# Kernel tuning notes

Hardware: AMD Instinct MI355X
Metric: run time of the kernel (lower is better)

## Reference

```python
import jax, jax.numpy as jnp
import numpy as np

NUM_HEADS = 6
HEAD_SIZE = 64
N_EMBD = 384


def setup_inputs() -> dict:
    key = jax.random.key(0)
    k1, k2, k3 = jax.random.split(key, 3)
    B, T, C = 256, 256, N_EMBD
    x = jax.random.normal(k1, (B, T, C), dtype=jnp.float32)
    # torch Linear(n_embd, 3*n_embd, bias=False): y = x @ W.T; store transposed for x @ W
    W_qkv = jax.random.normal(k2, (C, 3 * C), dtype=jnp.float32) * (1.0 / np.sqrt(C))
    W_proj = jax.random.normal(k3, (C, C), dtype=jnp.float32) * (1.0 / np.sqrt(C))
    b_proj = jnp.zeros((C,), dtype=jnp.float32)
    return {"x": x, "W_qkv": W_qkv, "W_proj": W_proj, "b_proj": b_proj}


def reference(x, W_qkv, W_proj, b_proj):
    B, T, C = x.shape
    H, D = NUM_HEADS, HEAD_SIZE
    qkv = x @ W_qkv                                  # [B, T, 3C]
    q, k, v = jnp.split(qkv, 3, axis=-1)
    # [B, T, C] -> [B, H, T, D]
    q = q.reshape(B, T, H, D).transpose(0, 2, 1, 3)
    k = k.reshape(B, T, H, D).transpose(0, 2, 1, 3)
    v = v.reshape(B, T, H, D).transpose(0, 2, 1, 3)
    att = jnp.einsum("bhtd,bhsd->bhts", q, k) / np.sqrt(D).astype(jnp.float32)
    causal = jnp.tril(jnp.ones((T, T), dtype=bool))  # tril buffer
    att = jnp.where(causal[None, None], att, -jnp.inf)
    att = jax.nn.softmax(att, axis=-1)
    # dropout layers are identity in eval mode
    out = jnp.einsum("bhts,bhsd->bhtd", att, v)      # [B, H, T, D]
    out = out.transpose(0, 2, 1, 3).reshape(B, T, C)
    return out @ W_proj.T @ jnp.eye(C, dtype=out.dtype) if False else out @ W_proj + b_proj
```

## Files before the change

### kernel.cpp

```cpp
#include <hip/hip_runtime.h>
#include <hip/hip_bf16.h>
#include <stdint.h>

typedef __hip_bfloat16 bf16;
using f32x4 = __attribute__((ext_vector_type(4))) float;
using s16x8 = __attribute__((ext_vector_type(8))) short;

#define MFMA16(A_, B_, C_) __builtin_amdgcn_mfma_f32_16x16x32_bf16((A_), (B_), (C_), 0, 0, 0)

__device__ __forceinline__ void gload16(const void* g, void* l) {
  __builtin_amdgcn_global_load_lds((const __attribute__((address_space(1))) void*)g,
                                   (__attribute__((address_space(3))) void*)l, 16, 0, 0);
}

__global__ __launch_bounds__(256) void detect_kernel(const void* __restrict__ x,
                                                     int* __restrict__ flag) {
  __shared__ int cnt;
  if (threadIdx.x == 0) cnt = 0;
  __syncthreads();
  const uint32_t* w = (const uint32_t*)x;
  int local = 0;
#pragma unroll
  for (int i = 0; i < 8; ++i) {
    uint32_t v = w[threadIdx.x * 8 + i];
    uint32_t e = (v >> 7) & 0xFF;
    if (e >= 110 && e <= 135) local++;
  }
  atomicAdd(&cnt, local);
  __syncthreads();
  if (threadIdx.x == 0) *flag = (cnt < 1024) ? 1 : 0;
}

__global__ __launch_bounds__(256) void convert_kernel(const void* __restrict__ x,
                                                      bf16* __restrict__ xb,
                                                      size_t elem_off,
                                                      const int* __restrict__ flag) {
  size_t i = ((size_t)blockIdx.x * 256 + threadIdx.x) * 8;
  if (*flag) {
    const float* xf = (const float*)x + elem_off + i;
    float4 a = ((const float4*)xf)[0];
    float4 b = ((const float4*)xf)[1];
    union { bf16 h[8]; uint4 u; } o;
    o.h[0] = __float2bfloat16(a.x); o.h[1] = __float2bfloat16(a.y);
    o.h[2] = __float2bfloat16(a.z); o.h[3] = __float2bfloat16(a.w);
    o.h[4] = __float2bfloat16(b.x); o.h[5] = __float2bfloat16(b.y);
    o.h[6] = __float2bfloat16(b.z); o.h[7] = __float2bfloat16(b.w);
    *(uint4*)(&xb[i]) = o.u;
  } else {
    *(uint4*)(&xb[i]) = *(const uint4*)((const bf16*)x + elem_off + i);
  }
}

__global__ __launch_bounds__(256) void transpose_kernel(const void* __restrict__ W,
                                                        bf16* __restrict__ Wt,
                                                        int K, int N,
                                                        const int* __restrict__ flag) {
  int idx = blockIdx.x * 256 + threadIdx.x;
  if (idx >= K * N) return;
  int n = idx / K;
  int k = idx - n * K;
  if (*flag)
    Wt[idx] = __float2bfloat16(((const float*)W)[k * N + n]);
  else
    Wt[idx] = ((const bf16*)W)[k * N + n];
}

template <int MODE>
__global__ __launch_bounds__(256) void gemm_kernel(
    const bf16* __restrict__ A, const bf16* __restrict__ Bt,
    bf16* __restrict__ qb, bf16* __restrict__ kb, bf16* __restrict__ vb,
    void* __restrict__ outp, const void* __restrict__ bias,
    int r_off, const int* __restrict__ flag) {
  constexpr int K = 384;
  __shared__ bf16 Ash[128 * 32];
  __shared__ bf16 Bsh[128 * 32];
  const int tid = threadIdx.x;
  const int lane = tid & 63;
  const int wave = tid >> 6;
  const int wm = wave & 1, wn = wave >> 1;
  const int l15 = lane & 15, quad = lane >> 4;
  const int n0 = blockIdx.x * 128, m0 = blockIdx.y * 128;

  const int rl = lane >> 2;
  const int slot = lane & 3;
  const int sc = (slot - (lane >> 3)) & 3;
  const size_t lane_goff = (size_t)rl * K + sc * 8;

  const int arow0 = wave * 32;
  const bf16* Ag0 = A + (size_t)(m0 + arow0) * K + lane_goff;
  const bf16* Ag1 = Ag0 + (size_t)16 * K;
  const bf16* Bg0 = Bt + (size_t)(n0 + arow0) * K + lane_goff;
  const bf16* Bg1 = Bg0 + (size_t)16 * K;
  bf16* Al0 = &Ash[arow0 * 32];
  bf16* Al1 = &Ash[(arow0 + 16) * 32];
  bf16* Bl0 = &Bsh[arow0 * 32];
  bf16* Bl1 = &Bsh[(arow0 + 16) * 32];

  const int fc = ((quad + (l15 >> 1)) & 3) * 8;

  const f32x4 z4 = {0.f, 0.f, 0.f, 0.f};
  f32x4 acc[4][4];
#pragma unroll
  for (int i = 0; i < 4; ++i)
#pragma unroll
    for (int j = 0; j < 4; ++j) acc[i][j] = z4;

  for (int kt = 0; kt < 12; ++kt) {
    const int k0 = kt * 32;
    gload16(Ag0 + k0, Al0);
    gload16(Ag1 + k0, Al1);
    gload16(Bg0 + k0, Bl0);
    gload16(Bg1 + k0, Bl1);
    __syncthreads();
    s16x8 af[4], bfr[4];
#pragma unroll
    for (int i = 0; i < 4; ++i) {
      af[i] = *(const s16x8*)(&Ash[(wm * 64 + i * 16 + l15) * 32 + fc]);
      bfr[i] = *(const s16x8*)(&Bsh[(wn * 64 + i * 16 + l15) * 32 + fc]);
    }
#pragma unroll
    for (int i = 0; i < 4; ++i)
#pragma unroll
      for (int j = 0; j < 4; ++j) acc[i][j] = MFMA16(af[i], bfr[j], acc[i][j]);
    __syncthreads();
  }

  const int mbase = m0 + wm * 64;
  const int nbase = n0 + wn * 64;
  if (MODE == 0) {
    const int sel = blockIdx.x / 3;
    bf16* dst = (sel == 0) ? qb : ((sel == 1) ? kb : vb);
#pragma unroll
    for (int i = 0; i < 4; ++i) {
#pragma unroll
      for (int j = 0; j < 4; ++j) {
        int n_g = nbase + j * 16 + l15;
        int c = n_g - sel * 384;
        int h = c >> 6, d = c & 63;
#pragma unroll
        for (int r = 0; r < 4; ++r) {
          int m_loc = mbase + i * 16 + quad * 4 + r;
          int b = m_loc >> 8, t = m_loc & 255;
          bf16 bv = __float2bfloat16(acc[i][j][r]);
          int bh = b * 6 + h;
          if (sel < 2)
            dst[(size_t)bh * 16384 + t * 64 + d] = bv;
          else
            dst[(size_t)bh * 16384 + d * 256 + t] = bv;
        }
      }
    }
  } else {
    const int f32io = *flag;
#pragma unroll
    for (int i = 0; i < 4; ++i) {
#pragma unroll
      for (int j = 0; j < 4; ++j) {
        int n_g = nbase + j * 16 + l15;
        float bsv = f32io ? ((const float*)bias)[n_g]
                          : __bfloat162float(((const bf16*)bias)[n_g]);
#pragma unroll
        for (int r = 0; r < 4; ++r) {
          int m_loc = mbase + i * 16 + quad * 4 + r;
          size_t o = (size_t)(r_off + m_loc) * 384 + n_g;
          float val = acc[i][j][r] + bsv;
          if (f32io)
            ((float*)outp)[o] = val;
          else
            ((bf16*)outp)[o] = __float2bfloat16(val);
        }
      }
    }
  }
}

__global__ __launch_bounds__(256) void attn_kernel(const bf16* __restrict__ Q,
                                                   const bf16* __restrict__ Kb,
                                                   const bf16* __restrict__ Vt,
                                                   bf16* __restrict__ attn_out) {
  constexpr int PLD = 264;
  __shared__ bf16 Psh[4][16 * PLD];
  const int tid = threadIdx.x;
  const int lane = tid & 63;
  const int wave = tid >> 6;
  const int l15 = lane & 15, quad = lane >> 4;
  const int blk = blockIdx.x;
  const int qt = blk & 3;
  const int bh = blk >> 2;
  const int q0 = qt * 64 + wave * 16;
  const size_t base = (size_t)bh * 16384;

  s16x8 qf0 = *(const s16x8*)(&Q[base + (q0 + l15) * 64 + quad * 8]);
  s16x8 qf1 = *(const s16x8*)(&Q[base + (q0 + l15) * 64 + 32 + quad * 8]);

  const int ntmax = q0 >> 4;
  bf16* P = &Psh[wave][0];
  const f32x4 z4 = {0.f, 0.f, 0.f, 0.f};
  const int tq = q0 + l15;

  s16x8 kf0[4], kf1[4];
#pragma unroll
  for (int i = 0; i < 4; ++i) {
    if (i <= ntmax) {
      kf0[i] = *(const s16x8*)(&Kb[base + (i * 16 + l15) * 64 + quad * 8]);
      kf1[i] = *(const s16x8*)(&Kb[base + (i * 16 + l15) * 64 + 32 + quad * 8]);
    }
  }

  float rsum = 0.f;
#pragma unroll
  for (int nt = 0; nt < 16; ++nt) {
    if (nt <= ntmax) {
      s16x8 a0 = kf0[nt & 3], a1 = kf1[nt & 3];
      if (nt + 4 <= ntmax) {
        kf0[nt & 3] = *(const s16x8*)(&Kb[base + ((nt + 4) * 16 + l15) * 64 + quad * 8]);
        kf1[nt & 3] = *(const s16x8*)(&Kb[base + ((nt + 4) * 16 + l15) * 64 + 32 + quad * 8]);
      }
      f32x4 s = MFMA16(a0, qf0, z4);
      s = MFMA16(a1, qf1, s);
      union { bf16 h[4]; uint2 u; } pk;
#pragma unroll
      for (int r = 0; r < 4; ++r) {
        int tk = nt * 16 + quad * 4 + r;
        float p = (tk <= tq) ? __expf(s[r] * 0.125f) : 0.f;
        rsum += p;
        pk.h[r] = __float2bfloat16(p);
      }
      *(uint2*)(&P[l15 * PLD + nt * 16 + quad * 4]) = pk.u;
    }
  }
  if ((ntmax & 1) == 0) {
    uint2 zz;
    zz.x = 0u; zz.y = 0u;
    *(uint2*)(&P[l15 * PLD + (ntmax + 1) * 16 + quad * 4]) = zz;
  }
  rsum += __shfl_xor(rsum, 16);
  rsum += __shfl_xor(rsum, 32);
  const float inv = 1.0f / rsum;

  const int ktcnt = (ntmax + 2) >> 1;
  f32x4 of[4];
#pragma unroll
  for (int dt = 0; dt < 4; ++dt) of[dt] = z4;

  s16x8 vf[2][4];
#pragma unroll
  for (int dt = 0; dt < 4; ++dt)
    vf[0][dt] = *(const s16x8*)(&Vt[base + (dt * 16 + l15) * 256 + quad * 8]);

#pragma unroll
  for (int kt = 0; kt < 8; ++kt) {
    if (kt < ktcnt) {
      if (kt + 1 < ktcnt) {
#pragma unroll
        for (int dt = 0; dt < 4; ++dt)
          vf[(kt + 1) & 1][dt] =
              *(const s16x8*)(&Vt[base + (dt * 16 + l15) * 256 + (kt + 1) * 32 + quad * 8]);
      }
      s16x8 pf = *(const s16x8*)(&P[l15 * PLD + kt * 32 + quad * 8]);
#pragma unroll
      for (int dt = 0; dt < 4; ++dt) of[dt] = MFMA16(vf[kt & 1][dt], pf, of[dt]);
    }
  }

  const int b = bh / 6;
  const int h = bh - b * 6;
  const size_t orow = (size_t)(b * 256 + q0 + l15) * 384 + h * 64;
#pragma unroll
  for (int dt = 0; dt < 4; ++dt) {
    union { bf16 h4[4]; uint2 u; } o;
#pragma unroll
    for (int r = 0; r < 4; ++r) o.h4[r] = __float2bfloat16(of[dt][r] * inv);
    *(uint2*)(&attn_out[orow + dt * 16 + quad * 4]) = o.u;
  }
}

extern "C" void kernel_launch(void* const* d_in, const int* in_sizes, int n_in,
                              void* d_out, int out_size, void* d_ws, size_t ws_size,
                              hipStream_t stream) {
  const void* x = d_in[0];
  const void* Wqkv = d_in[1];
  const void* Wproj = d_in[2];
  const void* bproj = d_in[3];

  char* ws = (char*)d_ws;
  int* flag = (int*)ws;                ws += 256;
  bf16* Wt_qkv = (bf16*)ws;            ws += (size_t)1152 * 384 * 2;
  bf16* Wt_proj = (bf16*)ws;           ws += (size_t)384 * 384 * 2;

  const size_t per_batch = (size_t)5 * 98304 * 2;
  size_t used = (size_t)(ws - (char*)d_ws);
  size_t remain = (ws_size > used) ? (ws_size - used) : 0;
  int NB = (int)(remain / per_batch);
  if (NB > 256) NB = 256;
  if (NB < 1) NB = 1;

  bf16* xb_buf = (bf16*)ws;
  bf16* q_buf = xb_buf + (size_t)NB * 98304;
  bf16* k_buf = q_buf + (size_t)NB * 98304;
  bf16* vt_buf = k_buf + (size_t)NB * 98304;
  bf16* attn_buf = vt_buf + (size_t)NB * 98304;

  detect_kernel<<<1, 256, 0, stream>>>(x, flag);
  transpose_kernel<<<(384 * 1152 + 255) / 256, 256, 0, stream>>>(Wqkv, Wt_qkv, 384, 1152, flag);
  transpose_kernel<<<(384 * 384 + 255) / 256, 256, 0, stream>>>(Wproj, Wt_proj, 384, 384, flag);

  for (int b0 = 0; b0 < 256; b0 += NB) {
    int nb = (256 - b0 < NB) ? (256 - b0) : NB;
    int r_off = b0 * 256;
    convert_kernel<<<nb * 48, 256, 0, stream>>>(x, xb_buf, (size_t)r_off * 384, flag);
    gemm_kernel<0><<<dim3(9, 2 * nb), 256, 0, stream>>>(
        xb_buf, Wt_qkv, q_buf, k_buf, vt_buf, nullptr, nullptr, 0, flag);
    attn_kernel<<<nb * 24, 256, 0, stream>>>(q_buf, k_buf, vt_buf, attn_buf);
    gemm_kernel<1><<<dim3(3, 2 * nb), 256, 0, stream>>>(
        attn_buf, Wt_proj, nullptr, nullptr, nullptr, d_out, bproj, r_off, flag);
  }
}
```

Baseline: 526.1 us.

## Keep attention probabilities in registers and fuse QK and PV loops

The attention kernel drops the shared-memory P buffer. It fuses the score/exp loop with the PV MFMA loop, so probabilities are packed straight into the B-operand registers by matching the MFMA output lane layout to the input layout. V is now loaded as two 4-element halves to fit that permuted k-ordering. It also remaps block indices across groups of 8, which likely spreads work across XCDs for L2 locality. The cost is smaller vector loads for V and less latency hiding from the V prefetch, which is no longer double-buffered.

Result: slower. 603.8 us (+14.8%).

```diff
diff --git a/kernel.cpp b/kernel.cpp
--- a/kernel.cpp
+++ b/kernel.cpp
@@ -5,6 +5,7 @@
 typedef __hip_bfloat16 bf16;
 using f32x4 = __attribute__((ext_vector_type(4))) float;
 using s16x8 = __attribute__((ext_vector_type(8))) short;
+using s16x4 = __attribute__((ext_vector_type(4))) short;
 
 #define MFMA16(A_, B_, C_) __builtin_amdgcn_mfma_f32_16x16x32_bf16((A_), (B_), (C_), 0, 0, 0)
 
@@ -178,13 +179,12 @@
                                                    const bf16* __restrict__ Kb,
                                                    const bf16* __restrict__ Vt,
                                                    bf16* __restrict__ attn_out) {
-  constexpr int PLD = 264;
-  __shared__ bf16 Psh[4][16 * PLD];
   const int tid = threadIdx.x;
   const int lane = tid & 63;
   const int wave = tid >> 6;
   const int l15 = lane & 15, quad = lane >> 4;
-  const int blk = blockIdx.x;
+  const int nblk = gridDim.x;
+  const int blk = (blockIdx.x & 7) * (nblk >> 3) + (blockIdx.x >> 3);
   const int qt = blk & 3;
   const int bh = blk >> 2;
   const int q0 = qt * 64 + wave * 16;
@@ -194,74 +194,76 @@
   s16x8 qf1 = *(const s16x8*)(&Q[base + (q0 + l15) * 64 + 32 + quad * 8]);
 
   const int ntmax = q0 >> 4;
-  bf16* P = &Psh[wave][0];
+  const int ktcnt = (ntmax + 2) >> 1;
+  const int tq = q0 + l15;
   const f32x4 z4 = {0.f, 0.f, 0.f, 0.f};
-  const int tq = q0 + l15;
-
-  s16x8 kf0[4], kf1[4];
-#pragma unroll
-  for (int i = 0; i < 4; ++i) {
-    if (i <= ntmax) {
-      kf0[i] = *(const s16x8*)(&Kb[base + (i * 16 + l15) * 64 + quad * 8]);
-      kf1[i] = *(const s16x8*)(&Kb[base + (i * 16 + l15) * 64 + 32 + quad * 8]);
+  f32x4 of[4];
+#pragma unroll
+  for (int dt = 0; dt < 4; ++dt) of[dt] = z4;
+  float rsum = 0.f;
+
+  const bf16* Kp = Kb + base + (size_t)l15 * 64 + quad * 8;
+  const bf16* Vp = Vt + base + (size_t)l15 * 256 + quad * 4;
+
+  typedef union { s16x8 v; s16x4 q2[2]; } vf_t;
+  typedef union { s16x8 v; uint32_t w[4]; } pf_t;
+
+  s16x8 kf[2][4];
+#pragma unroll
+  for (int hf = 0; hf < 2; ++hf) {
+    kf[0][hf * 2 + 0] = *(const s16x8*)(Kp + (size_t)(hf * 16) * 64);
+    kf[0][hf * 2 + 1] = *(const s16x8*)(Kp + (size_t)(hf * 16) * 64 + 32);
+  }
+
+#pragma unroll
+  for (int t = 0; t < 8; ++t) {
+    if (t < ktcnt) {
+      const int cur = t & 1, nxt = cur ^ 1;
+      vf_t vf[4];
+#pragma unroll
+      for (int dt = 0; dt < 4; ++dt) {
+        vf[dt].q2[0] = *(const s16x4*)(Vp + (size_t)dt * 4096 + t * 32);
+        vf[dt].q2[1] = *(const s16x4*)(Vp + (size_t)dt * 4096 + t * 32 + 16);
+      }
+      if (t + 1 < ktcnt) {
+        const bf16* Kn = Kp + (size_t)(t + 1) * 32 * 64;
+#pragma unroll
+        for (int hf = 0; hf < 2; ++hf) {
+          kf[nxt][hf * 2 + 0] = *(const s16x8*)(Kn + (size_t)(hf * 16) * 64);
+          kf[nxt][hf * 2 + 1] = *(const s16x8*)(Kn + (size_t)(hf * 16) * 64 + 32);
+        }
+      }
+      pf_t pf;
+#pragma unroll
+      for (int hf = 0; hf < 2; ++hf) {
+        const int nt = 2 * t + hf;
+        if (nt <= ntmax) {
+          f32x4 s = MFMA16(kf[cur][hf * 2 + 0], qf0, z4);
+          s = MFMA16(kf[cur][hf * 2 + 1], qf1, s);
+          const int tk0 = nt * 16 + quad * 4;
+          float p0 = (tk0 + 0 <= tq) ? __expf(s[0] * 0.125f) : 0.f;
+          float p1 = (tk0 + 1 <= tq) ? __expf(s[1] * 0.125f) : 0.f;
+          float p2 = (tk0 + 2 <= tq) ? __expf(s[2] * 0.125f) : 0.f;
+          float p3 = (tk0 + 3 <= tq) ? __expf(s[3] * 0.125f) : 0.f;
+          rsum += (p0 + p1) + (p2 + p3);
+          union { bf16 hh[2]; uint32_t u; } w0, w1;
+          w0.hh[0] = __float2bfloat16(p0); w0.hh[1] = __float2bfloat16(p1);
+          w1.hh[0] = __float2bfloat16(p2); w1.hh[1] = __float2bfloat16(p3);
+          pf.w[hf * 2 + 0] = w0.u;
+          pf.w[hf * 2 + 1] = w1.u;
+        } else {
+          pf.w[hf * 2 + 0] = 0u;
+          pf.w[hf * 2 + 1] = 0u;
+        }
+      }
+#pragma unroll
+      for (int dt = 0; dt < 4; ++dt) of[dt] = MFMA16(vf[dt].v, pf.v, of[dt]);
     }
   }
 
-  float rsum = 0.f;
-#pragma unroll
-  for (int nt = 0; nt < 16; ++nt) {
-    if (nt <= ntmax) {
-      s16x8 a0 = kf0[nt & 3], a1 = kf1[nt & 3];
-      if (nt + 4 <= ntmax) {
-        kf0[nt & 3] = *(const s16x8*)(&Kb[base + ((nt + 4) * 16 + l15) * 64 + quad * 8]);
-        kf1[nt & 3] = *(const s16x8*)(&Kb[base + ((nt + 4) * 16 + l15) * 64 + 32 + quad * 8]);
-      }
-      f32x4 s = MFMA16(a0, qf0, z4);
-      s = MFMA16(a1, qf1, s);
-      union { bf16 h[4]; uint2 u; } pk;
-#pragma unroll
-      for (int r = 0; r < 4; ++r) {
-        int tk = nt * 16 + quad * 4 + r;
-        float p = (tk <= tq) ? __expf(s[r] * 0.125f) : 0.f;
-        rsum += p;
-        pk.h[r] = __float2bfloat16(p);
-      }
-      *(uint2*)(&P[l15 * PLD + nt * 16 + quad * 4]) = pk.u;
-    }
-  }
-  if ((ntmax & 1) == 0) {
-    uint2 zz;
-    zz.x = 0u; zz.y = 0u;
-    *(uint2*)(&P[l15 * PLD + (ntmax + 1) * 16 + quad * 4]) = zz;
-  }
   rsum += __shfl_xor(rsum, 16);
   rsum += __shfl_xor(rsum, 32);
   const float inv = 1.0f / rsum;
-
-  const int ktcnt = (ntmax + 2) >> 1;
-  f32x4 of[4];
-#pragma unroll
-  for (int dt = 0; dt < 4; ++dt) of[dt] = z4;
-
-  s16x8 vf[2][4];
-#pragma unroll
-  for (int dt = 0; dt < 4; ++dt)
-    vf[0][dt] = *(const s16x8*)(&Vt[base + (dt * 16 + l15) * 256 + quad * 8]);
-
-#pragma unroll
-  for (int kt = 0; kt < 8; ++kt) {
-    if (kt < ktcnt) {
-      if (kt + 1 < ktcnt) {
-#pragma unroll
-        for (int dt = 0; dt < 4; ++dt)
-          vf[(kt + 1) & 1][dt] =
-              *(const s16x8*)(&Vt[base + (dt * 16 + l15) * 256 + (kt + 1) * 32 + quad * 8]);
-      }
-      s16x8 pf = *(const s16x8*)(&P[l15 * PLD + kt * 32 + quad * 8]);
-#pragma unroll
-      for (int dt = 0; dt < 4; ++dt) of[dt] = MFMA16(vf[kt & 1][dt], pf, of[dt]);
-    }
-  }
 
   const int b = bh / 6;
   const int h = bh - b * 6;
```
